# Kernel tuning notes

Hardware: AMD Instinct MI355X
Metric: run time of the kernel (lower is better)

The kernel has to match this reference:

```python
import jax, jax.numpy as jnp
import numpy as np

TEMPERATURE = 1.0
EPS = 1e-5
COS_EPS = 1e-8  # torch CosineSimilarity default eps
N_POS, N_NEG, D = 512, 512, 512


def setup_inputs() -> dict:
    key = jax.random.key(0)
    k1, k2, k3 = jax.random.split(key, 3)
    tensor_positive = jax.random.normal(k1, (N_POS, D), dtype=jnp.float32)
    tensor_negative = jax.random.normal(k2, (N_NEG, D), dtype=jnp.float32)
    # nn.Linear(512*3, 1), weight ~ N(0, 0.02^2), bias zeros
    linear_w = jax.random.normal(k3, (1, 3 * D), dtype=jnp.float32) * 0.02
    linear_b = jnp.zeros((1,), dtype=jnp.float32)
    return {"tensor_positive": tensor_positive, "tensor_negative": tensor_negative,
            "linear_w": linear_w, "linear_b": linear_b}


def _cos_matrix(a, b):
    # pairwise cosine similarity [Na, Nb], matching torch CosineSimilarity eps clamp
    an = a / jnp.maximum(jnp.linalg.norm(a, axis=-1, keepdims=True), COS_EPS)
    bn = b / jnp.maximum(jnp.linalg.norm(b, axis=-1, keepdims=True), COS_EPS)
    return an @ bn.T


def reference(tensor_positive, tensor_negative, linear_w, linear_b):
    pos, neg = tensor_positive, tensor_negative
    n_pos, d = pos.shape
    n_neg = neg.shape[0]

    # NCE part
    logit_n = jnp.exp(_cos_matrix(pos, neg) / TEMPERATURE)        # [N, M]
    deno_n = jnp.sum(logit_n, axis=-1)                            # [N]
    logit_p = jnp.exp(_cos_matrix(pos, pos) / TEMPERATURE)        # [N, N]
    loss = jnp.sum(-jnp.log(logit_p / (deno_n[:, None] + logit_p + EPS)))

    # Pairwise classifier: linear(cat([a, b, |a-b|])) decomposed as
    # a@w1 + b@w2 + |a-b|@w3 to avoid materializing the 3D concat.
    w = linear_w[0]
    w1, w2, w3 = w[:d], w[d:2 * d], w[2 * d:]
    allv = jnp.concatenate([pos, neg], axis=0)                    # [N+M, D]
    t1 = pos @ w1                                                 # [N]
    t2 = allv @ w2                                                # [N+M]
    diff = jnp.abs(pos[:, None, :] - allv[None, :, :])            # [N, N+M, D]
    t3 = jnp.einsum('nmd,d->nm', diff, w3)                        # [N, N+M]
    logits = t1[:, None] + t2[None, :] + t3 + linear_b[0]
    labels = jnp.concatenate([jnp.ones((n_pos,), jnp.float32),
                              jnp.zeros((n_neg,), jnp.float32)])  # [N+M]
    # BCE(sigmoid(logits), labels), stable form; per-i mean then sum over i
    bce = labels[None, :] * jax.nn.softplus(-logits) + (1.0 - labels[None, :]) * jax.nn.softplus(logits)
    loss = loss + jnp.sum(jnp.mean(bce, axis=1))
    return loss
```

## Files before the change

kernel.cpp:

```cpp
#include <hip/hip_runtime.h>
#include <math.h>

#define NPOS 512
#define DIM  512
#define NB   1024
#define EPSV 1e-5f
#define COS_EPS 1e-8f

#define OFF_INV  0
#define OFF_T1   1024
#define OFF_T2   1536
#define OFF_DENO 2560
#define OFF_COS  3072

__device__ __forceinline__ float softplus_f(float x) {
    return fmaxf(x, 0.f) + __logf(1.f + __expf(-fabsf(x)));
}

__global__ __launch_bounds__(256) void prep_kernel(
    const float* __restrict__ pos, const float* __restrict__ neg,
    const float* __restrict__ w, float* __restrict__ ws, float* __restrict__ out)
{
    int gtid = blockIdx.x * 256 + threadIdx.x;
    if (gtid == 0) out[0] = 0.f;
    if (gtid < NPOS) ws[OFF_DENO + gtid] = 0.f;
    int row  = gtid >> 6;
    int lane = threadIdx.x & 63;
    if (row >= NB) return;
    bool is_pos = row < NPOS;
    const float* r = is_pos ? pos + row * DIM : neg + (row - NPOS) * DIM;

    const float4* r4  = (const float4*)r + lane * 2;
    const float4* w14 = (const float4*)(w) + lane * 2;
    const float4* w24 = (const float4*)(w + DIM) + lane * 2;
    float4 a0 = r4[0],  a1 = r4[1];
    float4 u0 = w14[0], u1 = w14[1];
    float4 v0 = w24[0], v1 = w24[1];

    float ss  = a0.x*a0.x + a0.y*a0.y + a0.z*a0.z + a0.w*a0.w
              + a1.x*a1.x + a1.y*a1.y + a1.z*a1.z + a1.w*a1.w;
    float dw1 = a0.x*u0.x + a0.y*u0.y + a0.z*u0.z + a0.w*u0.w
              + a1.x*u1.x + a1.y*u1.y + a1.z*u1.z + a1.w*u1.w;
    float dw2 = a0.x*v0.x + a0.y*v0.y + a0.z*v0.z + a0.w*v0.w
              + a1.x*v1.x + a1.y*v1.y + a1.z*v1.z + a1.w*v1.w;

    #pragma unroll
    for (int off = 32; off; off >>= 1) {
        ss  += __shfl_xor(ss, off);
        dw1 += __shfl_xor(dw1, off);
        dw2 += __shfl_xor(dw2, off);
    }
    if (lane == 0) {
        float inv = 1.f / fmaxf(sqrtf(ss), COS_EPS);
        ws[OFF_INV + row] = inv;
        ws[OFF_T2 + row]  = dw2;
        if (is_pos) ws[OFF_T1 + row] = dw1;
    }
}

__global__ __launch_bounds__(256) void fused_kernel(
    const float* __restrict__ pos, const float* __restrict__ neg,
    const float* __restrict__ w, const float* __restrict__ lb,
    float* __restrict__ ws, float* __restrict__ out)
{
    __shared__ __align__(16) float As[32][36];
    __shared__ __align__(16) float Bs[64][36];
    __shared__ float red[4];

    const int tid = threadIdx.x;
    const int n0 = blockIdx.y * 32;
    const int m0 = blockIdx.x * 64;
    const bool isneg = (m0 >= NPOS);
    const float* Asrc = pos + (size_t)n0 * DIM;
    const float* Bsrc = isneg ? (neg + (size_t)(m0 - NPOS) * DIM)
                              : (pos + (size_t)m0 * DIM);
    const float* w3 = w + 2 * DIM;

    const int lr = tid >> 3;
    const int lc = (tid & 7) << 2;
    const int ti = tid >> 4;
    const int tj = tid & 15;

    float c[2][4] = {{0.f}}, t[2][4] = {{0.f}};

    float4 a0 = *(const float4*)(Asrc + lr * DIM + lc);
    float4 b0 = *(const float4*)(Bsrc + lr * DIM + lc);
    float4 b1 = *(const float4*)(Bsrc + (lr + 32) * DIM + lc);
    *(float4*)&As[lr][lc]      = a0;
    *(float4*)&Bs[lr][lc]      = b0;
    *(float4*)&Bs[lr + 32][lc] = b1;
    __syncthreads();

    #pragma unroll 1
    for (int iter = 0; iter < DIM / 32; ++iter) {
        const bool more = (iter < DIM / 32 - 1);
        if (more) {
            const float* ap = Asrc + (iter + 1) * 32;
            const float* bp = Bsrc + (iter + 1) * 32;
            a0 = *(const float4*)(ap + lr * DIM + lc);
            b0 = *(const float4*)(bp + lr * DIM + lc);
            b1 = *(const float4*)(bp + (lr + 32) * DIM + lc);
        }
        const float* w3i = w3 + iter * 32;
        #pragma unroll
        for (int k = 0; k < 32; k += 4) {
            float4 av[2], bv[4];
            #pragma unroll
            for (int r = 0; r < 2; ++r) av[r] = *(const float4*)&As[ti + 16 * r][k];
            #pragma unroll
            for (int s = 0; s < 4; ++s) bv[s] = *(const float4*)&Bs[tj + 16 * s][k];
            const float4 wv = *(const float4*)(w3i + k);
            #pragma unroll
            for (int r = 0; r < 2; ++r) {
                #pragma unroll
                for (int s = 0; s < 4; ++s) {
                    c[r][s] = fmaf(av[r].x, bv[s].x, c[r][s]);
                    c[r][s] = fmaf(av[r].y, bv[s].y, c[r][s]);
                    c[r][s] = fmaf(av[r].z, bv[s].z, c[r][s]);
                    c[r][s] = fmaf(av[r].w, bv[s].w, c[r][s]);
                    t[r][s] = fmaf(fabsf(av[r].x - bv[s].x), wv.x, t[r][s]);
                    t[r][s] = fmaf(fabsf(av[r].y - bv[s].y), wv.y, t[r][s]);
                    t[r][s] = fmaf(fabsf(av[r].z - bv[s].z), wv.z, t[r][s]);
                    t[r][s] = fmaf(fabsf(av[r].w - bv[s].w), wv.w, t[r][s]);
                }
            }
        }
        if (more) {
            __syncthreads();
            *(float4*)&As[lr][lc]      = a0;
            *(float4*)&Bs[lr][lc]      = b0;
            *(float4*)&Bs[lr + 32][lc] = b1;
            __syncthreads();
        }
    }

    const float bias = lb[0];
    float inv_n[2], t1_n[2], inv_m[4], t2_m[4];
    #pragma unroll
    for (int r = 0; r < 2; ++r) {
        int n = n0 + ti + 16 * r;
        inv_n[r] = ws[OFF_INV + n];
        t1_n[r]  = ws[OFF_T1 + n];
    }
    #pragma unroll
    for (int s = 0; s < 4; ++s) {
        int m = m0 + tj + 16 * s;
        inv_m[s] = ws[OFF_INV + m];
        t2_m[s]  = ws[OFF_T2 + m];
    }

    float bce = 0.f;
    float rowsum[2] = {0.f, 0.f};
    #pragma unroll
    for (int r = 0; r < 2; ++r) {
        #pragma unroll
        for (int s = 0; s < 4; ++s) {
            float cc = c[r][s] * inv_n[r] * inv_m[s];
            float lg = t1_n[r] + t2_m[s] + t[r][s] + bias;
            bce += softplus_f(isneg ? lg : -lg);
            if (isneg) {
                rowsum[r] += __expf(cc);
            } else {
                int n = n0 + ti + 16 * r;
                int m = m0 + tj + 16 * s;
                ws[OFF_COS + (size_t)n * NPOS + m] = cc;
            }
        }
    }

    if (isneg) {
        #pragma unroll
        for (int off = 1; off < 16; off <<= 1) {
            rowsum[0] += __shfl_xor(rowsum[0], off);
            rowsum[1] += __shfl_xor(rowsum[1], off);
        }
        if (tj == 0) {
            atomicAdd(&ws[OFF_DENO + n0 + ti], rowsum[0]);
            atomicAdd(&ws[OFF_DENO + n0 + ti + 16], rowsum[1]);
        }
    }

    #pragma unroll
    for (int off = 32; off; off >>= 1) bce += __shfl_xor(bce, off);
    const int lane = tid & 63, wid = tid >> 6;
    if (lane == 0) red[wid] = bce;
    __syncthreads();
    if (tid == 0)
        atomicAdd(out, (red[0] + red[1] + red[2] + red[3]) * (1.f / 1024.f));
}

__global__ __launch_bounds__(128) void finish_kernel(
    float* __restrict__ ws, float* __restrict__ out)
{
    const int n = blockIdx.x * 2 + (threadIdx.x >> 6);
    const int l = threadIdx.x & 63;
    const float4* C = (const float4*)(ws + OFF_COS + (size_t)n * NPOS);
    const float deno = ws[OFF_DENO + n];

    float part = 0.f;
    #pragma unroll
    for (int j = 0; j < 2; ++j) {
        float4 cc = C[l + 64 * j];
        part += __logf(deno + __expf(cc.x) + EPSV) - cc.x;
        part += __logf(deno + __expf(cc.y) + EPSV) - cc.y;
        part += __logf(deno + __expf(cc.z) + EPSV) - cc.z;
        part += __logf(deno + __expf(cc.w) + EPSV) - cc.w;
    }

    #pragma unroll
    for (int off = 32; off; off >>= 1) part += __shfl_xor(part, off);
    if (l == 0) atomicAdd(out, part);
}

extern "C" void kernel_launch(void* const* d_in, const int* in_sizes, int n_in,
                              void* d_out, int out_size, void* d_ws, size_t ws_size,
                              hipStream_t stream) {
    (void)in_sizes; (void)n_in; (void)out_size; (void)ws_size;
    const float* pos = (const float*)d_in[0];
    const float* neg = (const float*)d_in[1];
    const float* w   = (const float*)d_in[2];
    const float* lb  = (const float*)d_in[3];
    float* out = (float*)d_out;
    float* ws  = (float*)d_ws;

    prep_kernel<<<256, 256, 0, stream>>>(pos, neg, w, ws, out);
    fused_kernel<<<dim3(16, 16), 256, 0, stream>>>(pos, neg, w, lb, ws, out);
    finish_kernel<<<256, 128, 0, stream>>>(ws, out);
}
```

Baseline: 108.6 us.

## Halve fused kernel tile width and double-buffer shared memory tiles

```diff
diff --git a/kernel.cpp b/kernel.cpp
--- a/kernel.cpp
+++ b/kernel.cpp
@@ -63,13 +63,13 @@
     const float* __restrict__ w, const float* __restrict__ lb,
     float* __restrict__ ws, float* __restrict__ out)
 {
-    __shared__ __align__(16) float As[32][36];
-    __shared__ __align__(16) float Bs[64][36];
+    __shared__ __align__(16) float As[2][32][36];
+    __shared__ __align__(16) float Bs[2][32][36];
     __shared__ float red[4];
 
     const int tid = threadIdx.x;
     const int n0 = blockIdx.y * 32;
-    const int m0 = blockIdx.x * 64;
+    const int m0 = blockIdx.x * 32;
     const bool isneg = (m0 >= NPOS);
     const float* Asrc = pos + (size_t)n0 * DIM;
     const float* Bsrc = isneg ? (neg + (size_t)(m0 - NPOS) * DIM)
@@ -81,61 +81,56 @@
     const int ti = tid >> 4;
     const int tj = tid & 15;
 
-    float c[2][4] = {{0.f}}, t[2][4] = {{0.f}};
+    float c[2][2] = {{0.f}}, t[2][2] = {{0.f}};
 
     float4 a0 = *(const float4*)(Asrc + lr * DIM + lc);
     float4 b0 = *(const float4*)(Bsrc + lr * DIM + lc);
-    float4 b1 = *(const float4*)(Bsrc + (lr + 32) * DIM + lc);
-    *(float4*)&As[lr][lc]      = a0;
-    *(float4*)&Bs[lr][lc]      = b0;
-    *(float4*)&Bs[lr + 32][lc] = b1;
+    *(float4*)&As[0][lr][lc] = a0;
+    *(float4*)&Bs[0][lr][lc] = b0;
     __syncthreads();
 
     #pragma unroll 1
     for (int iter = 0; iter < DIM / 32; ++iter) {
+        const int cur = iter & 1;
         const bool more = (iter < DIM / 32 - 1);
         if (more) {
             const float* ap = Asrc + (iter + 1) * 32;
             const float* bp = Bsrc + (iter + 1) * 32;
             a0 = *(const float4*)(ap + lr * DIM + lc);
             b0 = *(const float4*)(bp + lr * DIM + lc);
-            b1 = *(const float4*)(bp + (lr + 32) * DIM + lc);
         }
         const float* w3i = w3 + iter * 32;
         #pragma unroll
         for (int k = 0; k < 32; k += 4) {
-            float4 av[2], bv[4];
-            #pragma unroll
-            for (int r = 0; r < 2; ++r) av[r] = *(const float4*)&As[ti + 16 * r][k];
-            #pragma unroll
-            for (int s = 0; s < 4; ++s) bv[s] = *(const float4*)&Bs[tj + 16 * s][k];
+            float4 av0 = *(const float4*)&As[cur][ti][k];
+            float4 av1 = *(const float4*)&As[cur][ti + 16][k];
+            float4 bv0 = *(const float4*)&Bs[cur][tj][k];
+            float4 bv1 = *(const float4*)&Bs[cur][tj + 16][k];
             const float4 wv = *(const float4*)(w3i + k);
-            #pragma unroll
-            for (int r = 0; r < 2; ++r) {
-                #pragma unroll
-                for (int s = 0; s < 4; ++s) {
-                    c[r][s] = fmaf(av[r].x, bv[s].x, c[r][s]);
-                    c[r][s] = fmaf(av[r].y, bv[s].y, c[r][s]);
-                    c[r][s] = fmaf(av[r].z, bv[s].z, c[r][s]);
-                    c[r][s] = fmaf(av[r].w, bv[s].w, c[r][s]);
-                    t[r][s] = fmaf(fabsf(av[r].x - bv[s].x), wv.x, t[r][s]);
-                    t[r][s] = fmaf(fabsf(av[r].y - bv[s].y), wv.y, t[r][s]);
-                    t[r][s] = fmaf(fabsf(av[r].z - bv[s].z), wv.z, t[r][s]);
-                    t[r][s] = fmaf(fabsf(av[r].w - bv[s].w), wv.w, t[r][s]);
-                }
-            }
+            #define ACC(r, s, AV, BV) \
+                c[r][s] = fmaf(AV.x, BV.x, c[r][s]); \
+                c[r][s] = fmaf(AV.y, BV.y, c[r][s]); \
+                c[r][s] = fmaf(AV.z, BV.z, c[r][s]); \
+                c[r][s] = fmaf(AV.w, BV.w, c[r][s]); \
+                t[r][s] = fmaf(fabsf(AV.x - BV.x), wv.x, t[r][s]); \
+                t[r][s] = fmaf(fabsf(AV.y - BV.y), wv.y, t[r][s]); \
+                t[r][s] = fmaf(fabsf(AV.z - BV.z), wv.z, t[r][s]); \
+                t[r][s] = fmaf(fabsf(AV.w - BV.w), wv.w, t[r][s]);
+            ACC(0, 0, av0, bv0)
+            ACC(0, 1, av0, bv1)
+            ACC(1, 0, av1, bv0)
+            ACC(1, 1, av1, bv1)
+            #undef ACC
         }
         if (more) {
+            *(float4*)&As[cur ^ 1][lr][lc] = a0;
+            *(float4*)&Bs[cur ^ 1][lr][lc] = b0;
             __syncthreads();
-            *(float4*)&As[lr][lc]      = a0;
-            *(float4*)&Bs[lr][lc]      = b0;
-            *(float4*)&Bs[lr + 32][lc] = b1;
-            __syncthreads();
         }
     }
 
     const float bias = lb[0];
-    float inv_n[2], t1_n[2], inv_m[4], t2_m[4];
+    float inv_n[2], t1_n[2], inv_m[2], t2_m[2];
     #pragma unroll
     for (int r = 0; r < 2; ++r) {
         int n = n0 + ti + 16 * r;
@@ -143,7 +138,7 @@
         t1_n[r]  = ws[OFF_T1 + n];
     }
     #pragma unroll
-    for (int s = 0; s < 4; ++s) {
+    for (int s = 0; s < 2; ++s) {
         int m = m0 + tj + 16 * s;
         inv_m[s] = ws[OFF_INV + m];
         t2_m[s]  = ws[OFF_T2 + m];
@@ -154,7 +149,7 @@
     #pragma unroll
     for (int r = 0; r < 2; ++r) {
         #pragma unroll
-        for (int s = 0; s < 4; ++s) {
+        for (int s = 0; s < 2; ++s) {
             float cc = c[r][s] * inv_n[r] * inv_m[s];
             float lg = t1_n[r] + t2_m[s] + t[r][s] + bias;
             bce += softplus_f(isneg ? lg : -lg);
@@ -224,6 +219,6 @@
     float* ws  = (float*)d_ws;
 
     prep_kernel<<<256, 256, 0, stream>>>(pos, neg, w, ws, out);
-    fused_kernel<<<dim3(16, 16), 256, 0, stream>>>(pos, neg, w, lb, ws, out);
+    fused_kernel<<<dim3(32, 16), 256, 0, stream>>>(pos, neg, w, lb, ws, out);
     finish_kernel<<<256, 128, 0, stream>>>(ws, out);
 }
```

Result: faster. 99.04 us (median of 2 runs) (-8.8%).

## Double-buffer shared tiles and halve block tile height to double grid size

Applied to the files above, without the earlier changes.

```diff
diff --git a/kernel.cpp b/kernel.cpp
--- a/kernel.cpp
+++ b/kernel.cpp
@@ -58,17 +58,17 @@
     }
 }
 
-__global__ __launch_bounds__(256) void fused_kernel(
+__global__ __launch_bounds__(128) void fused_kernel(
     const float* __restrict__ pos, const float* __restrict__ neg,
     const float* __restrict__ w, const float* __restrict__ lb,
     float* __restrict__ ws, float* __restrict__ out)
 {
-    __shared__ __align__(16) float As[32][36];
-    __shared__ __align__(16) float Bs[64][36];
-    __shared__ float red[4];
+    __shared__ __align__(16) float As[2][16][36];
+    __shared__ __align__(16) float Bs[2][64][36];
+    __shared__ float red[2];
 
     const int tid = threadIdx.x;
-    const int n0 = blockIdx.y * 32;
+    const int n0 = blockIdx.y * 16;
     const int m0 = blockIdx.x * 64;
     const bool isneg = (m0 >= NPOS);
     const float* Asrc = pos + (size_t)n0 * DIM;
@@ -85,51 +85,58 @@
 
     float4 a0 = *(const float4*)(Asrc + lr * DIM + lc);
     float4 b0 = *(const float4*)(Bsrc + lr * DIM + lc);
-    float4 b1 = *(const float4*)(Bsrc + (lr + 32) * DIM + lc);
-    *(float4*)&As[lr][lc]      = a0;
-    *(float4*)&Bs[lr][lc]      = b0;
-    *(float4*)&Bs[lr + 32][lc] = b1;
+    float4 b1 = *(const float4*)(Bsrc + (lr + 16) * DIM + lc);
+    float4 b2 = *(const float4*)(Bsrc + (lr + 32) * DIM + lc);
+    float4 b3 = *(const float4*)(Bsrc + (lr + 48) * DIM + lc);
+    *(float4*)&As[0][lr][lc]      = a0;
+    *(float4*)&Bs[0][lr][lc]      = b0;
+    *(float4*)&Bs[0][lr + 16][lc] = b1;
+    *(float4*)&Bs[0][lr + 32][lc] = b2;
+    *(float4*)&Bs[0][lr + 48][lc] = b3;
     __syncthreads();
 
     #pragma unroll 1
     for (int iter = 0; iter < DIM / 32; ++iter) {
+        const int cur = iter & 1;
         const bool more = (iter < DIM / 32 - 1);
         if (more) {
             const float* ap = Asrc + (iter + 1) * 32;
             const float* bp = Bsrc + (iter + 1) * 32;
             a0 = *(const float4*)(ap + lr * DIM + lc);
             b0 = *(const float4*)(bp + lr * DIM + lc);
-            b1 = *(const float4*)(bp + (lr + 32) * DIM + lc);
+            b1 = *(const float4*)(bp + (lr + 16) * DIM + lc);
+            b2 = *(const float4*)(bp + (lr + 32) * DIM + lc);
+            b3 = *(const float4*)(bp + (lr + 48) * DIM + lc);
         }
         const float* w3i = w3 + iter * 32;
         #pragma unroll
         for (int k = 0; k < 32; k += 4) {
-            float4 av[2], bv[4];
+            float4 av0 = *(const float4*)&As[cur][ti][k];
+            float4 av1 = *(const float4*)&As[cur][ti + 8][k];
+            float4 bv[4];
             #pragma unroll
-            for (int r = 0; r < 2; ++r) av[r] = *(const float4*)&As[ti + 16 * r][k];
-            #pragma unroll
-            for (int s = 0; s < 4; ++s) bv[s] = *(const float4*)&Bs[tj + 16 * s][k];
-            const float4 wv = *(const float4*)(w3i + k);
-            #pragma unroll
-            for (int r = 0; r < 2; ++r) {
-                #pragma unroll
-                for (int s = 0; s < 4; ++s) {
-                    c[r][s] = fmaf(av[r].x, bv[s].x, c[r][s]);
-                    c[r][s] = fmaf(av[r].y, bv[s].y, c[r][s]);
-                    c[r][s] = fmaf(av[r].z, bv[s].z, c[r][s]);
-                    c[r][s] = fmaf(av[r].w, bv[s].w, c[r][s]);
-                    t[r][s] = fmaf(fabsf(av[r].x - bv[s].x), wv.x, t[r][s]);
-                    t[r][s] = fmaf(fabsf(av[r].y - bv[s].y), wv.y, t[r][s]);
-                    t[r][s] = fmaf(fabsf(av[r].z - bv[s].z), wv.z, t[r][s]);
-                    t[r][s] = fmaf(fabsf(av[r].w - bv[s].w), wv.w, t[r][s]);
-                }
-            }
+            for (int s = 0; s < 4; ++s)
+                bv[s] = *(const float4*)&Bs[cur][tj + 16 * s][k];
+            const float4 wv4 = *(const float4*)(w3i + k);
+            #define ACC(r, s, AV) \
+                c[r][s] = fmaf(AV.x, bv[s].x, c[r][s]); \
+                c[r][s] = fmaf(AV.y, bv[s].y, c[r][s]); \
+                c[r][s] = fmaf(AV.z, bv[s].z, c[r][s]); \
+                c[r][s] = fmaf(AV.w, bv[s].w, c[r][s]); \
+                t[r][s] = fmaf(fabsf(AV.x - bv[s].x), wv4.x, t[r][s]); \
+                t[r][s] = fmaf(fabsf(AV.y - bv[s].y), wv4.y, t[r][s]); \
+                t[r][s] = fmaf(fabsf(AV.z - bv[s].z), wv4.z, t[r][s]); \
+                t[r][s] = fmaf(fabsf(AV.w - bv[s].w), wv4.w, t[r][s]);
+            ACC(0, 0, av0) ACC(0, 1, av0) ACC(0, 2, av0) ACC(0, 3, av0)
+            ACC(1, 0, av1) ACC(1, 1, av1) ACC(1, 2, av1) ACC(1, 3, av1)
+            #undef ACC
         }
         if (more) {
-            __syncthreads();
-            *(float4*)&As[lr][lc]      = a0;
-            *(float4*)&Bs[lr][lc]      = b0;
-            *(float4*)&Bs[lr + 32][lc] = b1;
+            *(float4*)&As[cur ^ 1][lr][lc]      = a0;
+            *(float4*)&Bs[cur ^ 1][lr][lc]      = b0;
+            *(float4*)&Bs[cur ^ 1][lr + 16][lc] = b1;
+            *(float4*)&Bs[cur ^ 1][lr + 32][lc] = b2;
+            *(float4*)&Bs[cur ^ 1][lr + 48][lc] = b3;
             __syncthreads();
         }
     }
@@ -138,7 +145,7 @@
     float inv_n[2], t1_n[2], inv_m[4], t2_m[4];
     #pragma unroll
     for (int r = 0; r < 2; ++r) {
-        int n = n0 + ti + 16 * r;
+        int n = n0 + ti + 8 * r;
         inv_n[r] = ws[OFF_INV + n];
         t1_n[r]  = ws[OFF_T1 + n];
     }
@@ -161,7 +168,7 @@
             if (isneg) {
                 rowsum[r] += __expf(cc);
             } else {
-                int n = n0 + ti + 16 * r;
+                int n = n0 + ti + 8 * r;
                 int m = m0 + tj + 16 * s;
                 ws[OFF_COS + (size_t)n * NPOS + m] = cc;
             }
@@ -176,7 +183,7 @@
         }
         if (tj == 0) {
             atomicAdd(&ws[OFF_DENO + n0 + ti], rowsum[0]);
-            atomicAdd(&ws[OFF_DENO + n0 + ti + 16], rowsum[1]);
+            atomicAdd(&ws[OFF_DENO + n0 + ti + 8], rowsum[1]);
         }
     }
 
@@ -185,8 +192,7 @@
     const int lane = tid & 63, wid = tid >> 6;
     if (lane == 0) red[wid] = bce;
     __syncthreads();
-    if (tid == 0)
-        atomicAdd(out, (red[0] + red[1] + red[2] + red[3]) * (1.f / 1024.f));
+    if (tid == 0) atomicAdd(out, (red[0] + red[1]) * (1.f / 1024.f));
 }
 
 __global__ __launch_bounds__(128) void finish_kernel(
@@ -224,6 +230,6 @@
     float* ws  = (float*)d_ws;
 
     prep_kernel<<<256, 256, 0, stream>>>(pos, neg, w, ws, out);
-    fused_kernel<<<dim3(16, 16), 256, 0, stream>>>(pos, neg, w, lb, ws, out);
+    fused_kernel<<<dim3(16, 32), 128, 0, stream>>>(pos, neg, w, lb, ws, out);
     finish_kernel<<<256, 128, 0, stream>>>(ws, out);
 }
```

Result: slower. 116.7 us (+7.4%).
